# Performance work log

Measured on AMD Instinct MI355X. Metric: run time of the kernel, lower is better.

## Reference

```python
import jax, jax.numpy as jnp
import numpy as np

R_MIN, R_MAX = 0.01, 0.6
H, W = 16, 32            # coarse polar grid (output glimpse size)
UR, UT = 10, 10          # upsampling factors (avg-pool window)
CH = 3                   # input channels
ALPHA = 2.0              # adp_alpha
B = 128
IMG = 224


def make_polar_grid():
    Hr, Wt = H * UR, W * UT
    r = np.exp(np.linspace(np.log(R_MIN), np.log(R_MAX), Hr))  # log_r=True
    theta = 2.0 * np.pi * np.arange(Wt) / Wt
    gx = r[:, None] * np.sin(theta)[None, :]   # grid[...,0] = r*sin
    gy = r[:, None] * np.cos(theta)[None, :]   # grid[...,1] = r*cos
    return jnp.asarray(np.stack([gx, gy], axis=-1).astype(np.float32))  # [Hr,Wt,2]


def conv2d(x, w, b):
    y = jax.lax.conv_general_dilated(x, w, (1, 1), 'VALID',
                                     dimension_numbers=('NCHW', 'OIHW', 'NCHW'))
    return y + b[None, :, None, None]


def maxpool2(x):
    return jax.lax.reduce_window(x, -jnp.inf, jax.lax.max,
                                 (1, 1, 2, 2), (1, 1, 2, 2), 'VALID')


def grid_sample_border(x, grid):
    # x: [B,C,Hi,Wi]; grid: [B,Hg,Wg,2] in [-1,1] (x,y); align_corners=False,
    # padding_mode='border' -> clamp float coords to [0, size-1] then bilinear.
    Bn, C, Hi, Wi = x.shape
    ix = jnp.clip(((grid[..., 0] + 1.0) * Wi - 1.0) * 0.5, 0.0, Wi - 1.0)
    iy = jnp.clip(((grid[..., 1] + 1.0) * Hi - 1.0) * 0.5, 0.0, Hi - 1.0)
    x0 = jnp.floor(ix); y0 = jnp.floor(iy)
    wx = (ix - x0)[:, None, :, :]  # [B,1,Hg,Wg]
    wy = (iy - y0)[:, None, :, :]
    x0i = x0.astype(jnp.int32); y0i = y0.astype(jnp.int32)
    x1i = jnp.minimum(x0i + 1, Wi - 1); y1i = jnp.minimum(y0i + 1, Hi - 1)

    def gather(img, yy, xx):  # img [C,Hi,Wi]; yy,xx [Hg,Wg]
        return img[:, yy, xx]  # [C,Hg,Wg]

    g = jax.vmap(gather)
    v00 = g(x, y0i, x0i); v01 = g(x, y0i, x1i)
    v10 = g(x, y1i, x0i); v11 = g(x, y1i, x1i)
    return (v00 * (1 - wx) * (1 - wy) + v01 * wx * (1 - wy)
            + v10 * (1 - wx) * wy + v11 * wx * wy)


def setup_inputs() -> dict:
    key = jax.random.key(0)
    ks = jax.random.split(key, 12)
    hid = int(16 * 0.5)  # fc hidden = 8
    inp = {
        'x': jax.random.normal(ks[0], (B, CH, IMG, IMG), jnp.float32),
        'l_t_prev': jax.random.uniform(ks[1], (B, 2), jnp.float32, -1.0, 1.0),
        'grid_2d': make_polar_grid(),
        'conv1_w': jax.random.normal(ks[2], (6, CH, 5, 5), jnp.float32) * 0.1,
        'conv1_b': jnp.zeros((6,), jnp.float32),
        'conv2_w': jax.random.normal(ks[3], (16, 6, 5, 5), jnp.float32) * 0.1,
        'conv2_b': jnp.zeros((16,), jnp.float32),
        'fc1_w': jax.random.normal(ks[4], (hid, 16), jnp.float32) * 0.2,
        'fc1_b': jnp.zeros((hid,), jnp.float32),
        'fc2_w': jax.random.normal(ks[5], (2, hid), jnp.float32) * 0.2,
        'fc2_b': jnp.zeros((2,), jnp.float32),
    }
    return inp


def reference(x, l_t_prev, grid_2d, conv1_w, conv1_b, conv2_w, conv2_b,
              fc1_w, fc1_b, fc2_w, fc2_b):
    # attention branch: conv -> maxpool -> conv -> global avg -> fc -> sigmoid
    br = conv2d(x, conv1_w, conv1_b)
    br = maxpool2(br)
    br = conv2d(br, conv2_w, conv2_b)
    br = br.mean(axis=(2, 3))                       # AdaptiveAvgPool2d(1) -> [B,16]
    h = jax.nn.relu(br @ fc1_w.T + fc1_b)
    weight = jax.nn.sigmoid(h @ fc2_w.T + fc2_b) * ALPHA   # [B,2]
    # attention-scaled polar grid
    grid = (l_t_prev[:, None, None, :] + grid_2d[None]) * weight[:, None, None, :]
    sampled = grid_sample_border(x, grid)           # [B,C,H*UR,W*UT]
    Bn, C = sampled.shape[:2]
    pooled = sampled.reshape(Bn, C, H, UR, W, UT).mean(axis=(3, 5))  # AvgPool[UR,UT]
    return weight, pooled
```

## Files before the change

### kernel.cpp

```cpp
#include <hip/hip_runtime.h>
#include <hip/hip_fp16.h>
#include <math.h>

#define IMG   224
#define PLANE (IMG * IMG)
#define POOL1 110
#define NB    128

#define WS_W1P_OFF  77824ull
#define WS_XI_OFF   81920ull
#define WS_XI_BYTES (128ull * PLANE * 8ull)
#define WS_NEED     (WS_XI_OFF + WS_XI_BYTES + 16ull)

typedef __attribute__((ext_vector_type(2))) _Float16 half2_t;
typedef __attribute__((ext_vector_type(8))) unsigned short ushort8;

static __device__ __forceinline__ float fdot2f(unsigned int a, unsigned int b, float c) {
#if __has_builtin(__builtin_amdgcn_fdot2)
  return __builtin_amdgcn_fdot2(__builtin_bit_cast(half2_t, a),
                                __builtin_bit_cast(half2_t, b), c, false);
#else
  float a0 = __half2float(__ushort_as_half((unsigned short)(a & 0xffff)));
  float a1 = __half2float(__ushort_as_half((unsigned short)(a >> 16)));
  float b0 = __half2float(__ushort_as_half((unsigned short)(b & 0xffff)));
  float b1 = __half2float(__ushort_as_half((unsigned short)(b >> 16)));
  return fmaf(a1, b1, fmaf(a0, b0, c));
#endif
}

static __device__ __forceinline__ float h2f(unsigned short u) {
  return __half2float(__ushort_as_half(u));
}

__global__ __launch_bounds__(128) void k0w_pack(
    const float* __restrict__ w1, unsigned int* __restrict__ w1p)
{
  const int t = threadIdx.x;
  if (t >= 90) return;
  const int ky = t % 5, r = t / 5, oc = r % 6, c = r / 6;
  const float* w = w1 + ((oc * 3 + c) * 5 + ky) * 5;
  unsigned int* o = w1p + t * 3;
  o[0] = __builtin_bit_cast(unsigned int, __builtin_amdgcn_cvt_pkrtz(w[0], w[1]));
  o[1] = __builtin_bit_cast(unsigned int, __builtin_amdgcn_cvt_pkrtz(w[2], w[3]));
  o[2] = __builtin_bit_cast(unsigned int, w[4]);
}

__global__ __launch_bounds__(256) void k1_conv1(
    const float* __restrict__ x, const unsigned int* __restrict__ w1p,
    const float* __restrict__ b1, float* __restrict__ S,
    ushort4* __restrict__ xi, const int write_xi)
{
  const int tid = threadIdx.x;
  const int tile = blockIdx.x;
  const int b = blockIdx.y;
  const int t_y = tile / 7, t_x = tile % 7;
  const int P0y = t_y * 16, P0x = t_x * 16;
  const int ty = tid >> 4, tx = tid & 15;
  const int py = P0y + ty, px = P0x + tx;
  const bool xedge = (t_x == 0) || (t_x == 6);

  __shared__ _Float16 in_t[3][36][40];
  __shared__ float rp[16][6][5];

  const int by = 2 * P0y, bx = 2 * P0x;
  #pragma unroll
  for (int dr = 0; dr < 3; ++dr) {
    const int row = ty + dr * 16;
    if (dr == 2 && row >= 36) continue;
    const int gy = min(by + row, IMG - 1);
    #pragma unroll
    for (int dc = 0; dc < 3; ++dc) {
      const int col = tx + dc * 16;
      if (dc == 2 && col >= 36) continue;
      const int gx = min(bx + col, IMG - 1);
      const float* src = x + ((size_t)(b * 3) * IMG + gy) * IMG + gx;
      #pragma unroll
      for (int c = 0; c < 3; ++c)
        in_t[c][row][col] = (_Float16)src[c * PLANE];
    }
  }
  __syncthreads();

  float acc[6][4];
  #pragma unroll
  for (int oc = 0; oc < 6; ++oc) {
    float bb = b1[oc];
    acc[oc][0] = bb; acc[oc][1] = bb; acc[oc][2] = bb; acc[oc][3] = bb;
  }
  unsigned int core_r0[3], core_r1[3];

  #pragma unroll 1
  for (int c = 0; c < 3; ++c) {
    const unsigned int* wc = w1p + c * 90;
    #pragma unroll
    for (int i = 0; i < 6; ++i) {
      const unsigned int* rowp =
          (const unsigned int*)&in_t[c][2 * ty + i][2 * tx];
      const unsigned int u0 = rowp[0], u1 = rowp[1], u2 = rowp[2];
      const unsigned int o1 = (u0 >> 16) | (u1 << 16);
      const unsigned int o3 = (u1 >> 16) | (u2 << 16);
      const float f4 = h2f((unsigned short)(u2 & 0xffff));
      const float f5 = h2f((unsigned short)(u2 >> 16));
      if (i == 0) { core_r0[c] = u0; }
      if (i == 1) { core_r1[c] = u0; }
      #pragma unroll
      for (int oc = 0; oc < 6; ++oc) {
        if (i <= 4) {
          const unsigned int* w = wc + (oc * 5 + i) * 3;
          const unsigned int w01 = w[0], w23 = w[1];
          const float w4 = __builtin_bit_cast(float, w[2]);
          acc[oc][0] = fdot2f(u0, w01, acc[oc][0]);
          acc[oc][0] = fdot2f(u1, w23, acc[oc][0]);
          acc[oc][0] = fmaf(f4, w4, acc[oc][0]);
          acc[oc][1] = fdot2f(o1, w01, acc[oc][1]);
          acc[oc][1] = fdot2f(o3, w23, acc[oc][1]);
          acc[oc][1] = fmaf(f5, w4, acc[oc][1]);
        }
        if (i >= 1) {
          const unsigned int* w = wc + (oc * 5 + (i - 1)) * 3;
          const unsigned int w01 = w[0], w23 = w[1];
          const float w4 = __builtin_bit_cast(float, w[2]);
          acc[oc][2] = fdot2f(u0, w01, acc[oc][2]);
          acc[oc][2] = fdot2f(u1, w23, acc[oc][2]);
          acc[oc][2] = fmaf(f4, w4, acc[oc][2]);
          acc[oc][3] = fdot2f(o1, w01, acc[oc][3]);
          acc[oc][3] = fdot2f(o3, w23, acc[oc][3]);
          acc[oc][3] = fmaf(f5, w4, acc[oc][3]);
        }
      }
    }
  }

  if (write_xi) {
    const int gy0 = by + 2 * ty, gx0 = bx + 2 * tx;
    ushort4* dst = xi + (size_t)b * PLANE + (size_t)gy0 * IMG + gx0;
    {
      uint4 pk;
      pk.x = (core_r0[0] & 0xffffu) | (core_r0[1] << 16);
      pk.y = (core_r0[2] & 0xffffu);
      pk.z = (core_r0[0] >> 16) | (core_r0[1] & 0xffff0000u);
      pk.w = (core_r0[2] >> 16);
      *(uint4*)dst = pk;
    }
    {
      uint4 pk;
      pk.x = (core_r1[0] & 0xffffu) | (core_r1[1] << 16);
      pk.y = (core_r1[2] & 0xffffu);
      pk.z = (core_r1[0] >> 16) | (core_r1[1] & 0xffff0000u);
      pk.w = (core_r1[2] >> 16);
      *(uint4*)(dst + IMG) = pk;
    }
  }

  const bool valid = (py < POOL1) && (px < POOL1);
  float z[6];
  #pragma unroll
  for (int oc = 0; oc < 6; ++oc) {
    float m = fmaxf(fmaxf(acc[oc][0], acc[oc][1]),
                    fmaxf(acc[oc][2], acc[oc][3]));
    z[oc] = valid ? m : 0.0f;
  }

  if (xedge) {
    #pragma unroll
    for (int oc = 0; oc < 6; ++oc) {
      #pragma unroll
      for (int kx = 0; kx < 5; ++kx) {
        float vv = (px >= kx && px <= 105 + kx) ? z[oc] : 0.0f;
        vv += __shfl_xor(vv, 1, 16);
        vv += __shfl_xor(vv, 2, 16);
        vv += __shfl_xor(vv, 4, 16);
        vv += __shfl_xor(vv, 8, 16);
        if (tx == 0) rp[ty][oc][kx] = vv;
      }
    }
  } else {
    #pragma unroll
    for (int oc = 0; oc < 6; ++oc) {
      float vv = z[oc];
      vv += __shfl_xor(vv, 1, 16);
      vv += __shfl_xor(vv, 2, 16);
      vv += __shfl_xor(vv, 4, 16);
      vv += __shfl_xor(vv, 8, 16);
      if (tx == 0) rp[ty][oc][0] = vv;
    }
  }
  __syncthreads();

  if (tid < 150) {
    int oc = tid / 25, r = tid % 25, ky = r / 5, kx = r % 5;
    const int kxi = xedge ? kx : 0;
    float s = 0.f;
    #pragma unroll
    for (int t = 0; t < 16; ++t) {
      int gpy = P0y + t;
      if (gpy >= ky && gpy <= 105 + ky) s += rp[t][oc][kxi];
    }
    atomicAdd(&S[b * 150 + tid], s);
  }
}

__global__ __launch_bounds__(128) void k2_head(
    const float* __restrict__ S, const float* __restrict__ w2,
    const float* __restrict__ b2, const float* __restrict__ f1w,
    const float* __restrict__ f1b, const float* __restrict__ f2w,
    const float* __restrict__ f2b, float* __restrict__ wgt,
    float* __restrict__ out)
{
  const int b = threadIdx.x;
  if (b >= NB) return;

  float acc[16];
  #pragma unroll
  for (int oc = 0; oc < 16; ++oc) acc[oc] = 0.0f;
  for (int i = 0; i < 150; ++i) {
    float sv = S[b * 150 + i];
    #pragma unroll
    for (int oc = 0; oc < 16; ++oc)
      acc[oc] = fmaf(w2[oc * 150 + i], sv, acc[oc]);
  }
  const float inv = 1.0f / (106.0f * 106.0f);
  float br[16];
  #pragma unroll
  for (int oc = 0; oc < 16; ++oc) br[oc] = b2[oc] + acc[oc] * inv;

  float h[8];
  #pragma unroll
  for (int j = 0; j < 8; ++j) {
    float t = f1b[j];
    #pragma unroll
    for (int oc = 0; oc < 16; ++oc) t = fmaf(br[oc], f1w[j * 16 + oc], t);
    h[j] = fmaxf(t, 0.0f);
  }
  #pragma unroll
  for (int k = 0; k < 2; ++k) {
    float t = f2b[k];
    #pragma unroll
    for (int j = 0; j < 8; ++j) t = fmaf(h[j], f2w[k * 8 + j], t);
    float w = 2.0f / (1.0f + expf(-t));
    wgt[2 * b + k] = w;
    out[2 * b + k] = w;
  }
}

__global__ __launch_bounds__(320) void k3_sector(
    const ushort4* __restrict__ xi, const float* __restrict__ lprev,
    const float* __restrict__ g2d, const float* __restrict__ wgt,
    float* __restrict__ out)
{
  const int s = blockIdx.x;
  const int b = blockIdx.y;
  const int tid = threadIdx.x;
  const int cc = tid % 10;
  const int chunk = tid / 10;
  const int h = chunk >> 1;

  __shared__ float part[16 * 3];
  if (tid < 48) part[tid] = 0.0f;

  const float lx = lprev[2 * b],  ly = lprev[2 * b + 1];
  const float wx = wgt[2 * b],    wy = wgt[2 * b + 1];
  const float axx = 112.0f * wx, bxx = fmaf(lx, axx, 111.5f);
  const float ayy = 112.0f * wy, byy = fmaf(ly, ayy, 111.5f);
  const int col = s * 10 + cc;
  const int r0 = chunk * 5;
  const unsigned short* xbs = (const unsigned short*)(xi + (size_t)b * PLANE);
  const float2* gp = (const float2*)g2d;
  __syncthreads();

  float a0 = 0.f, a1 = 0.f, a2 = 0.f;
  #pragma unroll
  for (int j = 0; j < 5; ++j) {
    const float2 g = gp[(r0 + j) * 320 + col];
    float ix = fminf(fmaxf(fmaf(g.x, axx, bxx), 0.0f), 223.0f);
    float iy = fminf(fmaxf(fmaf(g.y, ayy, byy), 0.0f), 223.0f);
    float x0f = floorf(ix), y0f = floorf(iy);
    float fx = ix - x0f, fy = iy - y0f;
    int x0 = (int)x0f, y0 = (int)y0f;
    int y1 = min(y0 + 1, IMG - 1);
    ushort8 t, u;
    __builtin_memcpy(&t, xbs + 4 * (y0 * IMG + x0), 16);
    __builtin_memcpy(&u, xbs + 4 * (y1 * IMG + x0), 16);
    float w00 = (1.f - fx) * (1.f - fy), w01 = fx * (1.f - fy);
    float w10 = (1.f - fx) * fy,         w11 = fx * fy;
    a0 += w00 * h2f(t[0]) + w01 * h2f(t[4]) + w10 * h2f(u[0]) + w11 * h2f(u[4]);
    a1 += w00 * h2f(t[1]) + w01 * h2f(t[5]) + w10 * h2f(u[1]) + w11 * h2f(u[5]);
    a2 += w00 * h2f(t[2]) + w01 * h2f(t[6]) + w10 * h2f(u[2]) + w11 * h2f(u[6]);
  }
  atomicAdd(&part[h * 3 + 0], a0);
  atomicAdd(&part[h * 3 + 1], a1);
  atomicAdd(&part[h * 3 + 2], a2);
  __syncthreads();

  if (tid < 48) {
    const int hh = tid / 3, c = tid - hh * 3;
    out[256 + (((b * 3 + c) * 16 + hh) * 32) + s] = part[tid] * 0.01f;
  }
}

__global__ __launch_bounds__(320, 4) void k3_fallback(
    const float* __restrict__ x, const float* __restrict__ lprev,
    const float* __restrict__ g2d, const float* __restrict__ wgt,
    float* __restrict__ out)
{
  const int s = blockIdx.x;
  const int b = blockIdx.y;
  const int tid = threadIdx.x;
  const int cc = tid % 10;
  const int chunk = tid / 10;
  const int h = chunk >> 1;

  __shared__ float part[16 * 3];
  if (tid < 48) part[tid] = 0.0f;

  const float lx = lprev[2 * b],  ly = lprev[2 * b + 1];
  const float wx = wgt[2 * b],    wy = wgt[2 * b + 1];
  const int col = s * 10 + cc;
  const int r0 = chunk * 5;
  const float* xb = x + (size_t)b * 3 * PLANE;
  const float* p0 = xb;
  const float* p1 = xb + PLANE;
  const float* p2 = xb + 2 * PLANE;
  const float2* gp = (const float2*)g2d;
  __syncthreads();

  float a0 = 0.f, a1 = 0.f, a2 = 0.f;
  #pragma unroll
  for (int j = 0; j < 5; ++j) {
    const int rr = r0 + j;
    const float2 g = gp[rr * 320 + col];
    float gx = (lx + g.x) * wx;
    float gy = (ly + g.y) * wy;
    float ix = ((gx + 1.0f) * 224.0f - 1.0f) * 0.5f;
    float iy = ((gy + 1.0f) * 224.0f - 1.0f) * 0.5f;
    ix = fminf(fmaxf(ix, 0.0f), 223.0f);
    iy = fminf(fmaxf(iy, 0.0f), 223.0f);
    float x0f = floorf(ix), y0f = floorf(iy);
    float fx = ix - x0f, fy = iy - y0f;
    int x0 = (int)x0f, y0 = (int)y0f;
    int x1 = min(x0 + 1, IMG - 1), y1 = min(y0 + 1, IMG - 1);
    float w00 = (1.f - fx) * (1.f - fy), w01 = fx * (1.f - fy);
    float w10 = (1.f - fx) * fy,         w11 = fx * fy;
    int o00 = y0 * IMG + x0, o01 = y0 * IMG + x1;
    int o10 = y1 * IMG + x0, o11 = y1 * IMG + x1;
    a0 += w00 * p0[o00] + w01 * p0[o01] + w10 * p0[o10] + w11 * p0[o11];
    a1 += w00 * p1[o00] + w01 * p1[o01] + w10 * p1[o10] + w11 * p1[o11];
    a2 += w00 * p2[o00] + w01 * p2[o01] + w10 * p2[o10] + w11 * p2[o11];
  }
  atomicAdd(&part[h * 3 + 0], a0);
  atomicAdd(&part[h * 3 + 1], a1);
  atomicAdd(&part[h * 3 + 2], a2);
  __syncthreads();

  if (tid < 48) {
    const int hh = tid / 3, c = tid - hh * 3;
    out[256 + (((b * 3 + c) * 16 + hh) * 32) + s] = part[tid] * 0.01f;
  }
}

extern "C" void kernel_launch(void* const* d_in, const int* in_sizes, int n_in,
                              void* d_out, int out_size, void* d_ws, size_t ws_size,
                              hipStream_t stream) {
  const float* x     = (const float*)d_in[0];
  const float* lprev = (const float*)d_in[1];
  const float* g2d   = (const float*)d_in[2];
  const float* w1    = (const float*)d_in[3];
  const float* b1    = (const float*)d_in[4];
  const float* w2    = (const float*)d_in[5];
  const float* b2    = (const float*)d_in[6];
  const float* f1w   = (const float*)d_in[7];
  const float* f1b   = (const float*)d_in[8];
  const float* f2w   = (const float*)d_in[9];
  const float* f2b   = (const float*)d_in[10];
  float* out = (float*)d_out;

  float* S   = (float*)d_ws;
  float* wgt = S + NB * 150;
  unsigned int* w1p = (unsigned int*)((char*)d_ws + WS_W1P_OFF);
  ushort4* xi = (ushort4*)((char*)d_ws + WS_XI_OFF);

  const bool fast = (ws_size >= WS_NEED);

  hipMemsetAsync(d_ws, 0, NB * 150 * sizeof(float), stream);
  k0w_pack<<<1, 128, 0, stream>>>(w1, w1p);
  k1_conv1<<<dim3(49, NB), 256, 0, stream>>>(x, w1p, b1, S, xi, fast ? 1 : 0);
  k2_head<<<1, 128, 0, stream>>>(S, w2, b2, f1w, f1b, f2w, f2b, wgt, out);
  if (fast)
    k3_sector<<<dim3(32, NB), 320, 0, stream>>>(xi, lprev, g2d, wgt, out);
  else
    k3_fallback<<<dim3(32, NB), 320, 0, stream>>>(x, lprev, g2d, wgt, out);
}
```

Measured before the change: 157.1 us.

## Fold memset into pack kernel, parallelize head per batch, coarsen sector blocks

Removes the separate memset by having extra blocks of the weight-pack kernel zero the accumulator buffer. The head kernel becomes one 64-thread block per batch item with a wave shuffle reduction, instead of a single block where each thread loops serially over 150 inputs. The sector kernel now handles four sectors per block, which cuts the block count by four but adds two barriers per sector and leaves fewer blocks to spread across the GPU.

```diff
diff --git a/kernel.cpp b/kernel.cpp
--- a/kernel.cpp
+++ b/kernel.cpp
@@ -32,17 +32,22 @@
   return __half2float(__ushort_as_half(u));
 }
 
-__global__ __launch_bounds__(128) void k0w_pack(
-    const float* __restrict__ w1, unsigned int* __restrict__ w1p)
+__global__ __launch_bounds__(256) void k0w_pack(
+    const float* __restrict__ w1, unsigned int* __restrict__ w1p,
+    float* __restrict__ S)
 {
   const int t = threadIdx.x;
-  if (t >= 90) return;
-  const int ky = t % 5, r = t / 5, oc = r % 6, c = r / 6;
-  const float* w = w1 + ((oc * 3 + c) * 5 + ky) * 5;
-  unsigned int* o = w1p + t * 3;
-  o[0] = __builtin_bit_cast(unsigned int, __builtin_amdgcn_cvt_pkrtz(w[0], w[1]));
-  o[1] = __builtin_bit_cast(unsigned int, __builtin_amdgcn_cvt_pkrtz(w[2], w[3]));
-  o[2] = __builtin_bit_cast(unsigned int, w[4]);
+  if (blockIdx.x == 0) {
+    if (t >= 90) return;
+    const int ky = t % 5, r = t / 5, oc = r % 6, c = r / 6;
+    const float* w = w1 + ((oc * 3 + c) * 5 + ky) * 5;
+    unsigned int* o = w1p + t * 3;
+    o[0] = __builtin_bit_cast(unsigned int, __builtin_amdgcn_cvt_pkrtz(w[0], w[1]));
+    o[1] = __builtin_bit_cast(unsigned int, __builtin_amdgcn_cvt_pkrtz(w[2], w[3]));
+    o[2] = __builtin_bit_cast(unsigned int, w[4]);
+  } else {
+    S[(blockIdx.x - 1) * 256 + t] = 0.0f;
+  }
 }
 
 __global__ __launch_bounds__(256) void k1_conv1(
@@ -200,46 +205,55 @@
   }
 }
 
-__global__ __launch_bounds__(128) void k2_head(
+__global__ __launch_bounds__(64) void k2_head(
     const float* __restrict__ S, const float* __restrict__ w2,
     const float* __restrict__ b2, const float* __restrict__ f1w,
     const float* __restrict__ f1b, const float* __restrict__ f2w,
     const float* __restrict__ f2b, float* __restrict__ wgt,
     float* __restrict__ out)
 {
-  const int b = threadIdx.x;
-  if (b >= NB) return;
+  const int b = blockIdx.x;
+  const int t = threadIdx.x;
 
   float acc[16];
   #pragma unroll
   for (int oc = 0; oc < 16; ++oc) acc[oc] = 0.0f;
-  for (int i = 0; i < 150; ++i) {
+  #pragma unroll 1
+  for (int i = t; i < 150; i += 64) {
     float sv = S[b * 150 + i];
     #pragma unroll
     for (int oc = 0; oc < 16; ++oc)
       acc[oc] = fmaf(w2[oc * 150 + i], sv, acc[oc]);
   }
-  const float inv = 1.0f / (106.0f * 106.0f);
-  float br[16];
-  #pragma unroll
-  for (int oc = 0; oc < 16; ++oc) br[oc] = b2[oc] + acc[oc] * inv;
-
-  float h[8];
-  #pragma unroll
-  for (int j = 0; j < 8; ++j) {
-    float t = f1b[j];
-    #pragma unroll
-    for (int oc = 0; oc < 16; ++oc) t = fmaf(br[oc], f1w[j * 16 + oc], t);
-    h[j] = fmaxf(t, 0.0f);
-  }
-  #pragma unroll
-  for (int k = 0; k < 2; ++k) {
-    float t = f2b[k];
-    #pragma unroll
-    for (int j = 0; j < 8; ++j) t = fmaf(h[j], f2w[k * 8 + j], t);
-    float w = 2.0f / (1.0f + expf(-t));
-    wgt[2 * b + k] = w;
-    out[2 * b + k] = w;
+  #pragma unroll
+  for (int d = 1; d < 64; d <<= 1) {
+    #pragma unroll
+    for (int oc = 0; oc < 16; ++oc)
+      acc[oc] += __shfl_xor(acc[oc], d, 64);
+  }
+
+  if (t == 0) {
+    const float inv = 1.0f / (106.0f * 106.0f);
+    float br[16];
+    #pragma unroll
+    for (int oc = 0; oc < 16; ++oc) br[oc] = b2[oc] + acc[oc] * inv;
+    float h[8];
+    #pragma unroll
+    for (int j = 0; j < 8; ++j) {
+      float tt = f1b[j];
+      #pragma unroll
+      for (int oc = 0; oc < 16; ++oc) tt = fmaf(br[oc], f1w[j * 16 + oc], tt);
+      h[j] = fmaxf(tt, 0.0f);
+    }
+    #pragma unroll
+    for (int k = 0; k < 2; ++k) {
+      float tt = f2b[k];
+      #pragma unroll
+      for (int j = 0; j < 8; ++j) tt = fmaf(h[j], f2w[k * 8 + j], tt);
+      float w = 2.0f / (1.0f + expf(-tt));
+      wgt[2 * b + k] = w;
+      out[2 * b + k] = w;
+    }
   }
 }
 
@@ -248,7 +262,7 @@
     const float* __restrict__ g2d, const float* __restrict__ wgt,
     float* __restrict__ out)
 {
-  const int s = blockIdx.x;
+  const int sgrp = blockIdx.x;
   const int b = blockIdx.y;
   const int tid = threadIdx.x;
   const int cc = tid % 10;
@@ -262,39 +276,44 @@
   const float wx = wgt[2 * b],    wy = wgt[2 * b + 1];
   const float axx = 112.0f * wx, bxx = fmaf(lx, axx, 111.5f);
   const float ayy = 112.0f * wy, byy = fmaf(ly, ayy, 111.5f);
-  const int col = s * 10 + cc;
   const int r0 = chunk * 5;
   const unsigned short* xbs = (const unsigned short*)(xi + (size_t)b * PLANE);
   const float2* gp = (const float2*)g2d;
   __syncthreads();
 
-  float a0 = 0.f, a1 = 0.f, a2 = 0.f;
-  #pragma unroll
-  for (int j = 0; j < 5; ++j) {
-    const float2 g = gp[(r0 + j) * 320 + col];
-    float ix = fminf(fmaxf(fmaf(g.x, axx, bxx), 0.0f), 223.0f);
-    float iy = fminf(fmaxf(fmaf(g.y, ayy, byy), 0.0f), 223.0f);
-    float x0f = floorf(ix), y0f = floorf(iy);
-    float fx = ix - x0f, fy = iy - y0f;
-    int x0 = (int)x0f, y0 = (int)y0f;
-    int y1 = min(y0 + 1, IMG - 1);
-    ushort8 t, u;
-    __builtin_memcpy(&t, xbs + 4 * (y0 * IMG + x0), 16);
-    __builtin_memcpy(&u, xbs + 4 * (y1 * IMG + x0), 16);
-    float w00 = (1.f - fx) * (1.f - fy), w01 = fx * (1.f - fy);
-    float w10 = (1.f - fx) * fy,         w11 = fx * fy;
-    a0 += w00 * h2f(t[0]) + w01 * h2f(t[4]) + w10 * h2f(u[0]) + w11 * h2f(u[4]);
-    a1 += w00 * h2f(t[1]) + w01 * h2f(t[5]) + w10 * h2f(u[1]) + w11 * h2f(u[5]);
-    a2 += w00 * h2f(t[2]) + w01 * h2f(t[6]) + w10 * h2f(u[2]) + w11 * h2f(u[6]);
-  }
-  atomicAdd(&part[h * 3 + 0], a0);
-  atomicAdd(&part[h * 3 + 1], a1);
-  atomicAdd(&part[h * 3 + 2], a2);
-  __syncthreads();
-
-  if (tid < 48) {
-    const int hh = tid / 3, c = tid - hh * 3;
-    out[256 + (((b * 3 + c) * 16 + hh) * 32) + s] = part[tid] * 0.01f;
+  #pragma unroll 1
+  for (int q = 0; q < 4; ++q) {
+    const int s = sgrp * 4 + q;
+    const int col = s * 10 + cc;
+    float a0 = 0.f, a1 = 0.f, a2 = 0.f;
+    #pragma unroll
+    for (int j = 0; j < 5; ++j) {
+      const float2 g = gp[(r0 + j) * 320 + col];
+      float ix = fminf(fmaxf(fmaf(g.x, axx, bxx), 0.0f), 223.0f);
+      float iy = fminf(fmaxf(fmaf(g.y, ayy, byy), 0.0f), 223.0f);
+      float x0f = floorf(ix), y0f = floorf(iy);
+      float fx = ix - x0f, fy = iy - y0f;
+      int x0 = (int)x0f, y0 = (int)y0f;
+      int y1 = min(y0 + 1, IMG - 1);
+      ushort8 t, u;
+      __builtin_memcpy(&t, xbs + 4 * (y0 * IMG + x0), 16);
+      __builtin_memcpy(&u, xbs + 4 * (y1 * IMG + x0), 16);
+      float w00 = (1.f - fx) * (1.f - fy), w01 = fx * (1.f - fy);
+      float w10 = (1.f - fx) * fy,         w11 = fx * fy;
+      a0 += w00 * h2f(t[0]) + w01 * h2f(t[4]) + w10 * h2f(u[0]) + w11 * h2f(u[4]);
+      a1 += w00 * h2f(t[1]) + w01 * h2f(t[5]) + w10 * h2f(u[1]) + w11 * h2f(u[5]);
+      a2 += w00 * h2f(t[2]) + w01 * h2f(t[6]) + w10 * h2f(u[2]) + w11 * h2f(u[6]);
+    }
+    atomicAdd(&part[h * 3 + 0], a0);
+    atomicAdd(&part[h * 3 + 1], a1);
+    atomicAdd(&part[h * 3 + 2], a2);
+    __syncthreads();
+    if (tid < 48) {
+      const int hh = tid / 3, c = tid - hh * 3;
+      out[256 + (((b * 3 + c) * 16 + hh) * 32) + s] = part[tid] * 0.01f;
+      part[tid] = 0.0f;
+    }
+    __syncthreads();
   }
 }
 
@@ -381,12 +400,11 @@
 
   const bool fast = (ws_size >= WS_NEED);
 
-  hipMemsetAsync(d_ws, 0, NB * 150 * sizeof(float), stream);
-  k0w_pack<<<1, 128, 0, stream>>>(w1, w1p);
+  k0w_pack<<<76, 256, 0, stream>>>(w1, w1p, S);
   k1_conv1<<<dim3(49, NB), 256, 0, stream>>>(x, w1p, b1, S, xi, fast ? 1 : 0);
-  k2_head<<<1, 128, 0, stream>>>(S, w2, b2, f1w, f1b, f2w, f2b, wgt, out);
+  k2_head<<<NB, 64, 0, stream>>>(S, w2, b2, f1w, f1b, f2w, f2b, wgt, out);
   if (fast)
-    k3_sector<<<dim3(32, NB), 320, 0, stream>>>(xi, lprev, g2d, wgt, out);
+    k3_sector<<<dim3(8, NB), 320, 0, stream>>>(xi, lprev, g2d, wgt, out);
   else
     k3_fallback<<<dim3(32, NB), 320, 0, stream>>>(x, lprev, g2d, wgt, out);
 }
```

New measurement: 127.1 us. 1.24x faster.
